# Performance work log

Measured on AMD Instinct MI355X. Metric: run time of the kernel, lower is better.

## Reference

```python
import jax, jax.numpy as jnp
import numpy as np

BATCH, NODES, CH_IN, CH_OUT, N_EXPERTS = 8, 8192, 128, 128, 64

def setup_inputs() -> dict:
    key = jax.random.key(0)
    kx, kw, ks = jax.random.split(key, 3)
    x = jax.random.normal(kx, (BATCH, NODES, CH_IN), dtype=jnp.float32)
    # std = fan_in**-0.5 per self_init
    W = jax.random.normal(kw, (N_EXPERTS, CH_OUT, CH_IN), dtype=jnp.float32) * (CH_IN ** -0.5)
    sel = jax.random.randint(ks, (NODES,), 0, N_EXPERTS, dtype=jnp.int64)
    return {"x": x, "sel": sel, "W": W}

def reference(x, sel, W):
    # x: (b, n, j), W[sel]: (n, i, j) -> out: (b, n, i)
    Wsel = W[sel]  # gather a (ch_out, ch_in) matrix per node
    return jnp.einsum('bnj,nij->bni', x, Wsel)
```

## Files before the change

kernel.cpp:

```cpp
#include <hip/hip_runtime.h>

#define BATCH   8
#define NODES   8192
#define CH      128
#define NEXP    64
#define TN      16
#define MAXP    (NODES + NEXP * TN)
#define NTILES  (MAXP / TN)
#define NSORT   64
#define SLICE   (NODES / NSORT)

typedef __attribute__((ext_vector_type(8))) short bf16x8;
typedef __attribute__((ext_vector_type(4))) float f32x4;

typedef const __attribute__((address_space(1))) unsigned int gu32;
typedef __attribute__((address_space(3))) unsigned int lu32;

__device__ __forceinline__ bf16x8 cvt8(f32x4 lo, f32x4 hi) {
    bf16x8 r;
    #pragma unroll
    for (int i = 0; i < 4; ++i) {
        r[i]     = (short)__builtin_bit_cast(unsigned short, static_cast<__bf16>(lo[i]));
        r[i + 4] = (short)__builtin_bit_cast(unsigned short, static_cast<__bf16>(hi[i]));
    }
    return r;
}

__global__ __launch_bounds__(256)
void prep1_kernel(const int* __restrict__ sel, const float* __restrict__ W,
                  short* __restrict__ Wbf, int* __restrict__ sorted,
                  int* __restrict__ texp, int* __restrict__ gcnt)
{
    const int t   = threadIdx.x;
    const int blk = blockIdx.x;

    #pragma unroll
    for (int i = 0; i < 2; ++i) {
        const int g8  = blk * 512 + i * 256 + t;
        const int e   = g8 >> 11;
        const int row = (g8 & 2047) >> 4;
        const int chk = g8 & 15;
        const float* ws = W + (size_t)g8 * 8;
        f32x4 lo = *reinterpret_cast<const f32x4*>(ws);
        f32x4 hi = *reinterpret_cast<const f32x4*>(ws + 4);
        short* wd = Wbf + ((size_t)e << 14) + row * CH + ((chk ^ (row & 7)) << 3);
        *reinterpret_cast<bf16x8*>(wd) = cvt8(lo, hi);
    }

    {
        const int si = blk * 256 + t;
        if (si < MAXP)   sorted[si] = -1;
        if (si < NTILES) texp[si]   = -1;
    }

    if (blk < NSORT) {
        __shared__ int hist[NEXP];
        if (t < NEXP) hist[t] = 0;
        __syncthreads();
        if (t < SLICE) atomicAdd(&hist[sel[blk * SLICE + t]], 1);
        __syncthreads();
        if (t < NEXP) gcnt[blk * NEXP + t] = hist[t];
    }
}

__global__ __launch_bounds__(128)
void prep2_kernel(const int* __restrict__ sel, const int* __restrict__ gcnt,
                  int* __restrict__ sorted, int* __restrict__ texp)
{
    const int t   = threadIdx.x;
    const int blk = blockIdx.x;

    __shared__ int cursor[NEXP];

    if (t < NEXP) {
        int cnt = 0, own = 0;
        #pragma unroll
        for (int s = 0; s < NSORT; ++s) {
            int g = gcnt[s * NEXP + t];
            own += (s < blk) ? g : 0;
            cnt += g;
        }
        int p = (cnt + TN - 1) & ~(TN - 1);
        int scan = p;
        #pragma unroll
        for (int d = 1; d < NEXP; d <<= 1) {
            int v = __shfl_up(scan, d);
            if (t >= d) scan += v;
        }
        cursor[t] = (scan - p) + own;
    }
    __syncthreads();

    if (t < SLICE) {
        int n = blk * SLICE + t;
        int e = sel[n];
        int pos = atomicAdd(&cursor[e], 1);
        sorted[pos] = n;
        if ((pos & (TN - 1)) == 0) texp[pos >> 4] = e;
    }
}

__global__ __launch_bounds__(256)
void gemm_kernel(const float* __restrict__ x, const short* __restrict__ Wbf,
                 float* __restrict__ out, const int* __restrict__ sorted,
                 const int* __restrict__ texp)
{
    __shared__ short s_w[CH * CH];

    const int tid  = threadIdx.x;
    const int tile = blockIdx.x;

    int e = texp[tile];
    if (e < 0) return;
    e = __builtin_amdgcn_readfirstlane(e);

    const int wave = tid >> 6;
    const int lane = tid & 63;
    const int m16  = lane & 15;
    const int quad = lane >> 4;

    {
        const char* gsrc = (const char*)(Wbf + ((size_t)e << 14))
                         + wave * 8192 + lane * 16;
        char* ldst = (char*)s_w + wave * 8192;
        #pragma unroll
        for (int i = 0; i < 8; ++i) {
            __builtin_amdgcn_global_load_lds(
                (gu32*)(gsrc + i * 1024),
                (lu32*)(ldst + i * 1024),
                16, 0, 0);
        }
    }

    int          nodej[2];
    const float* xrow[2];
    #pragma unroll
    for (int jt = 0; jt < 2; ++jt) {
        int j    = wave * 32 + jt * 16 + m16;
        int node = sorted[tile * TN + (j >> 3)];
        int b    = j & 7;
        nodej[jt] = node;
        int nd   = (node >= 0) ? node : 0;
        xrow[jt] = x + ((size_t)(b * NODES + nd)) * CH;
    }

    f32x4 xl[2][4][2];
    #pragma unroll
    for (int jt = 0; jt < 2; ++jt)
        #pragma unroll
        for (int kk = 0; kk < 4; ++kk) {
            const float* p = xrow[jt] + kk * 32 + quad * 8;
            xl[jt][kk][0] = __builtin_nontemporal_load(
                                reinterpret_cast<const f32x4*>(p));
            xl[jt][kk][1] = __builtin_nontemporal_load(
                                reinterpret_cast<const f32x4*>(p) + 1);
        }

    __syncthreads();

    bf16x8 xfrag[2][4];
    #pragma unroll
    for (int jt = 0; jt < 2; ++jt)
        #pragma unroll
        for (int kk = 0; kk < 4; ++kk)
            xfrag[jt][kk] = cvt8(xl[jt][kk][0], xl[jt][kk][1]);

    f32x4 acc[2][8];
    #pragma unroll
    for (int jt = 0; jt < 2; ++jt)
        #pragma unroll
        for (int ct = 0; ct < 8; ++ct)
            acc[jt][ct] = (f32x4){0.f, 0.f, 0.f, 0.f};

    #pragma unroll
    for (int kk = 0; kk < 4; ++kk) {
        #pragma unroll
        for (int ct = 0; ct < 8; ++ct) {
            const int row = ct * 16 + m16;
            const bf16x8 wfrag = *reinterpret_cast<const bf16x8*>(
                s_w + row * CH + (((kk * 4 + quad) ^ (row & 7)) << 3));
            acc[0][ct] = __builtin_amdgcn_mfma_f32_16x16x32_bf16(
                             wfrag, xfrag[0][kk], acc[0][ct], 0, 0, 0);
            acc[1][ct] = __builtin_amdgcn_mfma_f32_16x16x32_bf16(
                             wfrag, xfrag[1][kk], acc[1][ct], 0, 0, 0);
        }
    }

    #pragma unroll
    for (int jt = 0; jt < 2; ++jt) {
        int node = nodej[jt];
        if (node < 0) continue;
        int j = wave * 32 + jt * 16 + m16;
        int b = j & 7;
        float* orow = out + ((size_t)(b * NODES + node)) * CH;
        #pragma unroll
        for (int ct = 0; ct < 8; ++ct)
            __builtin_nontemporal_store(acc[jt][ct],
                reinterpret_cast<f32x4*>(orow + ct * 16 + quad * 4));
    }
}

extern "C" void kernel_launch(void* const* d_in, const int* in_sizes, int n_in,
                              void* d_out, int out_size, void* d_ws, size_t ws_size,
                              hipStream_t stream)
{
    const float* x   = (const float*)d_in[0];
    const int*   sel = (const int*)  d_in[1];
    const float* W   = (const float*)d_in[2];
    float*       out = (float*)d_out;

    short* Wbf    = (short*)d_ws;
    int*   sorted = (int*)((char*)d_ws + (size_t)NEXP * CH * CH * sizeof(short));
    int*   gcnt   = sorted + MAXP;
    int*   texp   = gcnt + NSORT * NEXP;

    prep1_kernel<<<256, 256, 0, stream>>>(sel, W, Wbf, sorted, texp, gcnt);
    prep2_kernel<<<NSORT, 128, 0, stream>>>(sel, gcnt, sorted, texp);
    gemm_kernel<<<NTILES, 256, 0, stream>>>(x, Wbf, out, sorted, texp);
}
```

Measured before the change: 108.7 us.

## Split each node tile across two blocks by batch half

The grouped GEMM grid is doubled, with each block handling one expert tile for half of the batch (4 of 8 batch rows). Each wave now computes one 16-row MFMA tile instead of two, which halves accumulator registers and raises the number of blocks available to fill the GPU. In exchange, every expert weight matrix is loaded into LDS twice as often. Nontemporal loads and stores are also replaced with ordinary cached accesses.

```diff
diff --git a/kernel.cpp b/kernel.cpp
--- a/kernel.cpp
+++ b/kernel.cpp
@@ -108,7 +108,8 @@
     __shared__ short s_w[CH * CH];
 
     const int tid  = threadIdx.x;
-    const int tile = blockIdx.x;
+    const int tile = blockIdx.x >> 1;
+    const int bh   = blockIdx.x & 1;
 
     int e = texp[tile];
     if (e < 0) return;
@@ -132,45 +133,30 @@
         }
     }
 
-    int          nodej[2];
-    const float* xrow[2];
+    const int j    = wave * 16 + m16;
+    const int node = sorted[tile * TN + (j >> 2)];
+    const int b    = bh * 4 + (j & 3);
+    const int nd   = (node >= 0) ? node : 0;
+    const float* xrow = x + ((size_t)(b * NODES + nd)) * CH;
+
+    f32x4 xl[4][2];
     #pragma unroll
-    for (int jt = 0; jt < 2; ++jt) {
-        int j    = wave * 32 + jt * 16 + m16;
-        int node = sorted[tile * TN + (j >> 3)];
-        int b    = j & 7;
-        nodej[jt] = node;
-        int nd   = (node >= 0) ? node : 0;
-        xrow[jt] = x + ((size_t)(b * NODES + nd)) * CH;
+    for (int kk = 0; kk < 4; ++kk) {
+        const float* p = xrow + kk * 32 + quad * 8;
+        xl[kk][0] = *reinterpret_cast<const f32x4*>(p);
+        xl[kk][1] = *reinterpret_cast<const f32x4*>(p + 4);
     }
-
-    f32x4 xl[2][4][2];
-    #pragma unroll
-    for (int jt = 0; jt < 2; ++jt)
-        #pragma unroll
-        for (int kk = 0; kk < 4; ++kk) {
-            const float* p = xrow[jt] + kk * 32 + quad * 8;
-            xl[jt][kk][0] = __builtin_nontemporal_load(
-                                reinterpret_cast<const f32x4*>(p));
-            xl[jt][kk][1] = __builtin_nontemporal_load(
-                                reinterpret_cast<const f32x4*>(p) + 1);
-        }
 
     __syncthreads();
 
-    bf16x8 xfrag[2][4];
+    bf16x8 xfrag[4];
     #pragma unroll
-    for (int jt = 0; jt < 2; ++jt)
-        #pragma unroll
-        for (int kk = 0; kk < 4; ++kk)
-            xfrag[jt][kk] = cvt8(xl[jt][kk][0], xl[jt][kk][1]);
+    for (int kk = 0; kk < 4; ++kk)
+        xfrag[kk] = cvt8(xl[kk][0], xl[kk][1]);
 
-    f32x4 acc[2][8];
+    f32x4 acc[8];
     #pragma unroll
-    for (int jt = 0; jt < 2; ++jt)
-        #pragma unroll
-        for (int ct = 0; ct < 8; ++ct)
-            acc[jt][ct] = (f32x4){0.f, 0.f, 0.f, 0.f};
+    for (int ct = 0; ct < 8; ++ct) acc[ct] = (f32x4){0.f, 0.f, 0.f, 0.f};
 
     #pragma unroll
     for (int kk = 0; kk < 4; ++kk) {
@@ -179,24 +165,16 @@
             const int row = ct * 16 + m16;
             const bf16x8 wfrag = *reinterpret_cast<const bf16x8*>(
                 s_w + row * CH + (((kk * 4 + quad) ^ (row & 7)) << 3));
-            acc[0][ct] = __builtin_amdgcn_mfma_f32_16x16x32_bf16(
-                             wfrag, xfrag[0][kk], acc[0][ct], 0, 0, 0);
-            acc[1][ct] = __builtin_amdgcn_mfma_f32_16x16x32_bf16(
-                             wfrag, xfrag[1][kk], acc[1][ct], 0, 0, 0);
+            acc[ct] = __builtin_amdgcn_mfma_f32_16x16x32_bf16(
+                          wfrag, xfrag[kk], acc[ct], 0, 0, 0);
         }
     }
 
-    #pragma unroll
-    for (int jt = 0; jt < 2; ++jt) {
-        int node = nodej[jt];
-        if (node < 0) continue;
-        int j = wave * 32 + jt * 16 + m16;
-        int b = j & 7;
+    if (node >= 0) {
         float* orow = out + ((size_t)(b * NODES + node)) * CH;
         #pragma unroll
         for (int ct = 0; ct < 8; ++ct)
-            __builtin_nontemporal_store(acc[jt][ct],
-                reinterpret_cast<f32x4*>(orow + ct * 16 + quad * 4));
+            *reinterpret_cast<f32x4*>(orow + ct * 16 + quad * 4) = acc[ct];
     }
 }
 
@@ -216,5 +194,5 @@
 
     prep1_kernel<<<256, 256, 0, stream>>>(sel, W, Wbf, sorted, texp, gcnt);
     prep2_kernel<<<NSORT, 128, 0, stream>>>(sel, gcnt, sorted, texp);
-    gemm_kernel<<<NTILES, 256, 0, stream>>>(x, Wbf, out, sorted, texp);
+    gemm_kernel<<<NTILES * 2, 256, 0, stream>>>(x, Wbf, out, sorted, texp);
 }
```

Measured after the change: 104.4 us. -3.9%, faster.
